# Performance work log

Measured on AMD Instinct MI355X. Metric: run time of the kernel, lower is better.

Reference implementation:

```python
import jax, jax.numpy as jnp
import numpy as np

N_NODES = 100000

def gcn_conv(x, src, dst, W, b, n):
    # PyG GCNConv: h = W x; add self-loops; norm = d^-1/2[src] * d^-1/2[dst]; scatter-add at dst; + b
    h = x @ W
    loop = jnp.arange(n, dtype=src.dtype)
    s = jnp.concatenate([src, loop])
    d = jnp.concatenate([dst, loop])
    deg = jax.ops.segment_sum(jnp.ones_like(d, dtype=h.dtype), d, num_segments=n)
    dis = jnp.where(deg > 0, jax.lax.rsqrt(deg), 0.0)
    norm = dis[s] * dis[d]                     # [E+n]
    msg = h[s] * norm[:, None]                  # [E+n, F] big gather
    out = jax.ops.segment_sum(msg, d, num_segments=n)
    return out + b

def setup_inputs() -> dict:
    key = jax.random.key(0)
    ks = jax.random.split(key, 12)
    n, e, f = N_NODES, 3200000, 14
    hid = [64, 64, 32]
    c = 2
    x = jax.random.normal(ks[0], (n, f), dtype=jnp.float32)
    edge_index = jax.random.randint(ks[1], (2, e), 0, n, dtype=jnp.int64)
    batch = jnp.sort(jax.random.randint(ks[2], (n,), 0, 2000, dtype=jnp.int64))
    def lin(k, fi, fo):
        s = 1.0 / np.sqrt(fi)
        return jax.random.uniform(k, (fi, fo), jnp.float32, -s, s)
    W1 = lin(ks[3], f, hid[0]); b1 = jnp.zeros((hid[0],), jnp.float32)
    W2 = lin(ks[4], hid[0], hid[1]); b2 = jnp.zeros((hid[1],), jnp.float32)
    W3 = lin(ks[5], hid[1], hid[2]); b3 = jnp.zeros((hid[2],), jnp.float32)
    W4 = lin(ks[6], hid[2], c); b4 = jnp.zeros((c,), jnp.float32)
    return {"x": x, "edge_index": edge_index, "batch": batch, "num_graphs": 2000,
            "W1": W1, "b1": b1, "W2": W2, "b2": b2, "W3": W3, "b3": b3, "W4": W4, "b4": b4}

def reference(x, edge_index, batch, num_graphs, W1, b1, W2, b2, W3, b3, W4, b4):
    n = x.shape[0]
    src, dst = edge_index[0], edge_index[1]
    h = jax.nn.relu(gcn_conv(x, src, dst, W1, b1, n))   # dropout = identity at inference
    h = jax.nn.relu(gcn_conv(h, src, dst, W2, b2, n))
    h = jax.nn.relu(gcn_conv(h, src, dst, W3, b3, n))
    h = gcn_conv(h, src, dst, W4, b4, n)
    # global mean pool over graphs
    sums = jax.ops.segment_sum(h, batch, num_segments=num_graphs)
    cnts = jax.ops.segment_sum(jnp.ones((n,), h.dtype), batch, num_segments=num_graphs)
    pooled = sums / jnp.maximum(cnts, 1.0)[:, None]
    return jax.nn.log_softmax(pooled, axis=-1)
```

## Files before the change

kernel.cpp:

```cpp
#include <hip/hip_runtime.h>
#include <hip/hip_fp16.h>
#include <math.h>
#include <type_traits>

static constexpr int THREADS = 256;
static constexpr int CAP   = 80;
static constexpr int BSH   = 9;
static constexpr int SUBS  = 4;
static constexpr int SUBN  = 128;
static constexpr int CAPB  = 17920;
static constexpr int MAXB  = 256;


__global__ void k_zero_i(int* __restrict__ p, int n) {
    int i = blockIdx.x * blockDim.x + threadIdx.x;
    if (i < n) p[i] = 0;
}


__global__ __launch_bounds__(THREADS)
void k_part(const int* __restrict__ src, const int* __restrict__ dst,
            int* __restrict__ bcnt, int* __restrict__ pairs, int e, int nbuck) {
    __shared__ int hist[MAXB];
    __shared__ int base_s[MAXB];
    for (int i = threadIdx.x; i < nbuck; i += THREADS) hist[i] = 0;
    __syncthreads();

    int i0 = (blockIdx.x * THREADS + (int)threadIdx.x) * 8;
    int ss[8], dd[8], bb[8], rk[8];
    int c8 = 0;
    if (i0 < e) {
        c8 = min(8, e - i0);
        if (c8 == 8) {
            int4 d0 = ((const int4*)(dst + i0))[0];
            int4 d1 = ((const int4*)(dst + i0))[1];
            int4 s0 = ((const int4*)(src + i0))[0];
            int4 s1 = ((const int4*)(src + i0))[1];
            dd[0]=d0.x; dd[1]=d0.y; dd[2]=d0.z; dd[3]=d0.w;
            dd[4]=d1.x; dd[5]=d1.y; dd[6]=d1.z; dd[7]=d1.w;
            ss[0]=s0.x; ss[1]=s0.y; ss[2]=s0.z; ss[3]=s0.w;
            ss[4]=s1.x; ss[5]=s1.y; ss[6]=s1.z; ss[7]=s1.w;
        } else {
            for (int j = 0; j < c8; ++j) { dd[j] = dst[i0 + j]; ss[j] = src[i0 + j]; }
        }
        for (int j = 0; j < c8; ++j) {
            bb[j] = dd[j] >> BSH;
            rk[j] = atomicAdd(&hist[bb[j]], 1);
        }
    }
    __syncthreads();
    for (int i = threadIdx.x; i < nbuck; i += THREADS)
        base_s[i] = hist[i] ? atomicAdd(&bcnt[i], hist[i]) : 0;
    __syncthreads();
    for (int j = 0; j < c8; ++j) {
        int idx = base_s[bb[j]] + rk[j];
        if (idx < CAPB)
            pairs[(size_t)bb[j] * CAPB + idx] = ((dd[j] & ((1 << BSH) - 1)) << 17) | ss[j];
    }
}


__global__ __launch_bounds__(THREADS)
void k_scat2(const int* __restrict__ pairs, const int* __restrict__ bcnt,
             int* __restrict__ cnt, int* __restrict__ csr, int n) {
    __shared__ int slab[SUBN * CAP];
    __shared__ int lcnt[SUBN];
    int bucket = blockIdx.x / SUBS;
    int sub    = blockIdx.x % SUBS;
    int gnode0 = (bucket << BSH) + sub * SUBN;
    if (gnode0 >= n) return;
    for (int i = threadIdx.x; i < SUBN; i += THREADS) lcnt[i] = 0;
    __syncthreads();

    int m = min(bcnt[bucket], CAPB);
    const int* pp = pairs + (size_t)bucket * CAPB;
    for (int i0 = (int)threadIdx.x * 4; i0 < m; i0 += THREADS * 4) {
        int k = min(4, m - i0);
        int v[4];
        if (k == 4) {
            int4 a = *(const int4*)(pp + i0);
            v[0] = a.x; v[1] = a.y; v[2] = a.z; v[3] = a.w;
        } else {
            for (int j = 0; j < k; ++j) v[j] = pp[i0 + j];
        }
#pragma unroll
        for (int j = 0; j < 4; ++j) {
            if (j < k) {
                int dl = v[j] >> 17;
                if ((dl >> 7) == sub) {
                    int ln = dl & (SUBN - 1);
                    int p = atomicAdd(&lcnt[ln], 1);
                    if (p < CAP) slab[ln * CAP + p] = v[j] & 0x1FFFF;
                }
            }
        }
    }
    __syncthreads();

    size_t gbase = (size_t)gnode0 * CAP;
    for (int idx = threadIdx.x; idx < SUBN * CAP; idx += THREADS) {
        int node = gnode0 + idx / CAP;
        if (node < n) csr[gbase + idx] = slab[idx];
    }
    for (int i = threadIdx.x; i < SUBN; i += THREADS) {
        int node = gnode0 + i;
        if (node < n) cnt[node] = min(lcnt[i], CAP);
    }
}


__global__ __launch_bounds__(THREADS)
void k_dis_xs(const int* __restrict__ deg, const float* __restrict__ x,
              float* __restrict__ dis, __half2* __restrict__ xs, int n) {
    int i = blockIdx.x * blockDim.x + threadIdx.x;
    if (i >= n) return;
    float dn = rsqrtf((float)(deg[i] + 1));
    dis[i] = dn;
    const float* xr = x + (size_t)i * 14;
    __half2* o = xs + (size_t)i * 8;
#pragma unroll
    for (int fl = 0; fl < 7; ++fl) {
        float2 v;
        v.x = dn * xr[fl * 2];
        v.y = dn * xr[fl * 2 + 1];
        o[fl] = __float22half2_rn(v);
    }
    o[7] = __float22half2_rn(make_float2(0.f, 0.f));
}


template<int SG, int HPL, bool SELF_SCALE, bool EPI_SCALE, bool BIAS, bool RELU>
__global__ __launch_bounds__(THREADS)
void k_gather_pk(const __half2* __restrict__ hw, const int* __restrict__ deg,
                 const int* __restrict__ csr, const float* __restrict__ dis,
                 const float* __restrict__ bias, float* __restrict__ out, int n) {
    constexpr int RS = SG * HPL;
    int tid = blockIdx.x * THREADS + threadIdx.x;
    int node = tid / SG;
    int fl = tid % SG;
    if (node >= n) return;
    size_t o = (size_t)node * CAP;
    int dg = deg[node];
    float dn = dis[node];

    auto loadrow = [&](int s, __half2* r) {
        const __half2* p = hw + (size_t)s * RS + fl * HPL;
        if constexpr (HPL == 4) {
            union { uint4 u; __half2 h[4]; } t;
            t.u = *(const uint4*)p;
            r[0] = t.h[0]; r[1] = t.h[1]; r[2] = t.h[2]; r[3] = t.h[3];
        } else if constexpr (HPL == 2) {
            union { uint2 u; __half2 h[2]; } t;
            t.u = *(const uint2*)p;
            r[0] = t.h[0]; r[1] = t.h[1];
        } else {
            r[0] = *p;
        }
    };

    float2 self[HPL];
    {
        __half2 r[HPL];
        loadrow(node, r);
#pragma unroll
        for (int q = 0; q < HPL; ++q) {
            self[q] = __half22float2(r[q]);
            if (SELF_SCALE) { self[q].x *= dn; self[q].y *= dn; }
        }
    }

    __half2 z = __float2half2_rn(0.f);
    __half2 c0[HPL], c1[HPL], c2[HPL], c3[HPL];
#pragma unroll
    for (int q = 0; q < HPL; ++q) { c0[q] = z; c1[q] = z; c2[q] = z; c3[q] = z; }

    int base = 0;
    for (; base + SG <= dg; base += SG) {
        int cs = csr[o + base + fl];
#pragma unroll
        for (int t = 0; t < SG; t += 4) {
            int s0 = __shfl(cs, t, SG),     s1 = __shfl(cs, t + 1, SG);
            int s2 = __shfl(cs, t + 2, SG), s3 = __shfl(cs, t + 3, SG);
            __half2 r0[HPL], r1[HPL], r2[HPL], r3[HPL];
            loadrow(s0, r0); loadrow(s1, r1); loadrow(s2, r2); loadrow(s3, r3);
#pragma unroll
            for (int q = 0; q < HPL; ++q) {
                c0[q] = __hadd2(c0[q], r0[q]);
                c1[q] = __hadd2(c1[q], r1[q]);
                c2[q] = __hadd2(c2[q], r2[q]);
                c3[q] = __hadd2(c3[q], r3[q]);
            }
        }
    }
    int rem = dg - base;
    if (rem > 0) {
        int cs = (fl < rem) ? csr[o + base + fl] : 0;
        int t = 0;
        for (; t + 4 <= rem; t += 4) {
            int s0 = __shfl(cs, t, SG),     s1 = __shfl(cs, t + 1, SG);
            int s2 = __shfl(cs, t + 2, SG), s3 = __shfl(cs, t + 3, SG);
            __half2 r0[HPL], r1[HPL], r2[HPL], r3[HPL];
            loadrow(s0, r0); loadrow(s1, r1); loadrow(s2, r2); loadrow(s3, r3);
#pragma unroll
            for (int q = 0; q < HPL; ++q) {
                c0[q] = __hadd2(c0[q], r0[q]);
                c1[q] = __hadd2(c1[q], r1[q]);
                c2[q] = __hadd2(c2[q], r2[q]);
                c3[q] = __hadd2(c3[q], r3[q]);
            }
        }
        for (; t < rem; ++t) {
            int s = __shfl(cs, t, SG);
            __half2 r[HPL];
            loadrow(s, r);
#pragma unroll
            for (int q = 0; q < HPL; ++q) c0[q] = __hadd2(c0[q], r[q]);
        }
    }

    float* op = out + (size_t)node * 2 * RS + fl * 2 * HPL;
#pragma unroll
    for (int q = 0; q < HPL; ++q) {
        float2 v0 = __half22float2(c0[q]), v1 = __half22float2(c1[q]);
        float2 v2 = __half22float2(c2[q]), v3 = __half22float2(c3[q]);
        float2 v;
        v.x = self[q].x + (v0.x + v1.x) + (v2.x + v3.x);
        v.y = self[q].y + (v0.y + v1.y) + (v2.y + v3.y);
        if (EPI_SCALE) { v.x *= dn; v.y *= dn; }
        if (BIAS) {
            float2 b = ((const float2*)bias)[fl * HPL + q];
            v.x += b.x; v.y += b.y;
        }
        if (RELU) { v.x = fmaxf(v.x, 0.f); v.y = fmaxf(v.y, 0.f); }
        op[q * 2 + 0] = v.x;
        op[q * 2 + 1] = v.y;
    }
}


__global__ __launch_bounds__(THREADS)
void k_gather_l3(const __half2* __restrict__ hw, const int* __restrict__ deg,
                 const int* __restrict__ csr, const float* __restrict__ dis,
                 const float* __restrict__ b3, const float* __restrict__ W4,
                 float2* __restrict__ hw4, int n) {
    constexpr int SG = 4, HPL = 4, RS = 16;
    __shared__ float Ws4[64];
    if (threadIdx.x < 64) Ws4[threadIdx.x] = W4[threadIdx.x];
    __syncthreads();

    int tid = blockIdx.x * THREADS + threadIdx.x;
    int node = tid / SG;
    int fl = tid % SG;
    if (node >= n) return;
    size_t o = (size_t)node * CAP;
    int dg = deg[node];
    float dn = dis[node];

    auto loadrow = [&](int s, __half2* r) {
        union { uint4 u; __half2 h[4]; } t;
        t.u = *(const uint4*)(hw + (size_t)s * RS + fl * HPL);
        r[0] = t.h[0]; r[1] = t.h[1]; r[2] = t.h[2]; r[3] = t.h[3];
    };

    float2 self[HPL];
    {
        __half2 r[HPL];
        loadrow(node, r);
#pragma unroll
        for (int q = 0; q < HPL; ++q) self[q] = __half22float2(r[q]);
    }

    __half2 z = __float2half2_rn(0.f);
    __half2 c0[HPL], c1[HPL], c2[HPL], c3[HPL];
#pragma unroll
    for (int q = 0; q < HPL; ++q) { c0[q] = z; c1[q] = z; c2[q] = z; c3[q] = z; }

    int base = 0;
    for (; base + SG <= dg; base += SG) {
        int cs = csr[o + base + fl];
#pragma unroll
        for (int t = 0; t < SG; t += 4) {
            int s0 = __shfl(cs, t, SG),     s1 = __shfl(cs, t + 1, SG);
            int s2 = __shfl(cs, t + 2, SG), s3 = __shfl(cs, t + 3, SG);
            __half2 r0[HPL], r1[HPL], r2[HPL], r3[HPL];
            loadrow(s0, r0); loadrow(s1, r1); loadrow(s2, r2); loadrow(s3, r3);
#pragma unroll
            for (int q = 0; q < HPL; ++q) {
                c0[q] = __hadd2(c0[q], r0[q]);
                c1[q] = __hadd2(c1[q], r1[q]);
                c2[q] = __hadd2(c2[q], r2[q]);
                c3[q] = __hadd2(c3[q], r3[q]);
            }
        }
    }
    int rem = dg - base;
    if (rem > 0) {
        int cs = (fl < rem) ? csr[o + base + fl] : 0;
        for (int t = 0; t < rem; ++t) {
            int s = __shfl(cs, t, SG);
            __half2 r[HPL];
            loadrow(s, r);
#pragma unroll
            for (int q = 0; q < HPL; ++q) c0[q] = __hadd2(c0[q], r[q]);
        }
    }

    float p0 = 0.f, p1 = 0.f;
#pragma unroll
    for (int q = 0; q < HPL; ++q) {
        float2 v0 = __half22float2(c0[q]), v1 = __half22float2(c1[q]);
        float2 v2 = __half22float2(c2[q]), v3 = __half22float2(c3[q]);
        float2 v;
        v.x = self[q].x + (v0.x + v1.x) + (v2.x + v3.x);
        v.y = self[q].y + (v0.y + v1.y) + (v2.y + v3.y);
        v.x *= dn; v.y *= dn;
        float2 b = ((const float2*)b3)[fl * HPL + q];
        v.x = fmaxf(v.x + b.x, 0.f);
        v.y = fmaxf(v.y + b.y, 0.f);
        int f = 8 * fl + 2 * q;
        p0 += v.x * Ws4[f * 2 + 0] + v.y * Ws4[(f + 1) * 2 + 0];
        p1 += v.x * Ws4[f * 2 + 1] + v.y * Ws4[(f + 1) * 2 + 1];
    }
    p0 += __shfl_xor(p0, 1, SG); p0 += __shfl_xor(p0, 2, SG);
    p1 += __shfl_xor(p1, 1, SG); p1 += __shfl_xor(p1, 2, SG);
    if (fl == 0) hw4[node] = make_float2(p0 * dn, p1 * dn);
}


__global__ __launch_bounds__(THREADS)
void k_gather2p(const float2* __restrict__ hw, const int* __restrict__ deg,
                const int* __restrict__ csr, const float* __restrict__ dis,
                const float* __restrict__ b, const int* __restrict__ batch,
                float* __restrict__ sums, float* __restrict__ cnts, int n) {
    int tid = blockIdx.x * blockDim.x + threadIdx.x;
    int node = tid >> 3, fl = tid & 7;
    if (node >= n) return;
    size_t o = (size_t)node * CAP;
    int dg = deg[node];
    float x0 = 0.f, y0 = 0.f, x1 = 0.f, y1 = 0.f;
    for (int base = 0; base < dg; base += 32) {
        int idx0 = base + 4 * fl;
        int ldx = min(idx0, CAP - 4);
        int4 c4 = *(const int4*)(csr + o + ldx);
#pragma unroll
        for (int q = 0; q < 4; ++q) {
            bool ok = (idx0 + q) < dg;
            int s = ok ? (&c4.x)[q] : node;
            float2 v = hw[s];
            if (ok) {
                if (q & 1) { x1 += v.x; y1 += v.y; }
                else       { x0 += v.x; y0 += v.y; }
            }
        }
    }
    float sx = x0 + x1, sy = y0 + y1;
    sx += __shfl_xor(sx, 1, 8); sx += __shfl_xor(sx, 2, 8); sx += __shfl_xor(sx, 4, 8);
    sy += __shfl_xor(sy, 1, 8); sy += __shfl_xor(sy, 2, 8); sy += __shfl_xor(sy, 4, 8);
    if (fl == 0) {
        float2 a = hw[node];
        float dn = dis[node];
        float h0 = (a.x + sx) * dn + b[0];
        float h1 = (a.y + sy) * dn + b[1];
        int g = batch[node];
        atomicAdd(&sums[g * 2 + 0], h0);
        atomicAdd(&sums[g * 2 + 1], h1);
        atomicAdd(&cnts[g], 1.0f);
    }
}


template<int KW, int K, int KSTR, int FOUT, bool EPI_BIAS_RELU, typename OUT_T>
__global__ __launch_bounds__(THREADS)
void k_gemm_rb(const float* __restrict__ in, const float* __restrict__ W,
               const float* __restrict__ dis, const float* __restrict__ bias,
               OUT_T* __restrict__ out, int n) {
    constexpr int CG = FOUT / 4;
    __shared__ float Ws[K * FOUT];
    for (int i = threadIdx.x; i < K * FOUT; i += THREADS) {
        int r = i / FOUT;
        Ws[i] = (r < KW) ? W[i] : 0.0f;
    }
    __syncthreads();
    int gid = blockIdx.x * THREADS + threadIdx.x;
    int pair = gid / CG, cg = gid % CG;
    int node0 = pair * 2;
    if (node0 >= n) return;
    bool two = (node0 + 1 < n);
    const float4* r0 = (const float4*)(in + (size_t)node0 * KSTR);
    const float4* r1 = two ? (const float4*)(in + (size_t)(node0 + 1) * KSTR) : r0;
    const float4* Wf4 = (const float4*)Ws;
    float4 acc0 = {0.f, 0.f, 0.f, 0.f}, acc1 = {0.f, 0.f, 0.f, 0.f};
#pragma unroll
    for (int k0 = 0; k0 < K / 4; ++k0) {
        float4 x0 = r0[k0];
        float4 x1 = r1[k0];
#pragma unroll
        for (int kk = 0; kk < 4; ++kk) {
            float4 wv = Wf4[(k0 * 4 + kk) * CG + cg];
            float a = (&x0.x)[kk], b = (&x1.x)[kk];
            acc0.x += a * wv.x; acc0.y += a * wv.y; acc0.z += a * wv.z; acc0.w += a * wv.w;
            acc1.x += b * wv.x; acc1.y += b * wv.y; acc1.z += b * wv.z; acc1.w += b * wv.w;
        }
    }
    float dn0 = dis[node0];
    float dn1 = two ? dis[node0 + 1] : 0.f;
    acc0.x *= dn0; acc0.y *= dn0; acc0.z *= dn0; acc0.w *= dn0;
    acc1.x *= dn1; acc1.y *= dn1; acc1.z *= dn1; acc1.w *= dn1;
    if (EPI_BIAS_RELU) {
        float4 bv = ((const float4*)bias)[cg];
        acc0.x = fmaxf(acc0.x + bv.x, 0.f); acc0.y = fmaxf(acc0.y + bv.y, 0.f);
        acc0.z = fmaxf(acc0.z + bv.z, 0.f); acc0.w = fmaxf(acc0.w + bv.w, 0.f);
        acc1.x = fmaxf(acc1.x + bv.x, 0.f); acc1.y = fmaxf(acc1.y + bv.y, 0.f);
        acc1.z = fmaxf(acc1.z + bv.z, 0.f); acc1.w = fmaxf(acc1.w + bv.w, 0.f);
    }
    if constexpr (std::is_same<OUT_T, __half>::value) {
        union { __half2 h[2]; uint2 u; } p0, p1;
        p0.h[0] = __floats2half2_rn(acc0.x, acc0.y);
        p0.h[1] = __floats2half2_rn(acc0.z, acc0.w);
        *(uint2*)(out + (size_t)node0 * FOUT + cg * 4) = p0.u;
        if (two) {
            p1.h[0] = __floats2half2_rn(acc1.x, acc1.y);
            p1.h[1] = __floats2half2_rn(acc1.z, acc1.w);
            *(uint2*)(out + (size_t)(node0 + 1) * FOUT + cg * 4) = p1.u;
        }
    } else {
        ((float4*)(out + (size_t)node0 * FOUT))[cg] = acc0;
        if (two) ((float4*)(out + (size_t)(node0 + 1) * FOUT))[cg] = acc1;
    }
}


__global__ void k_zero2(float* __restrict__ sums, float* __restrict__ cnts, int ng) {
    int i = blockIdx.x * blockDim.x + threadIdx.x;
    if (i < ng) {
        sums[i * 2 + 0] = 0.0f;
        sums[i * 2 + 1] = 0.0f;
        cnts[i] = 0.0f;
    }
}

__global__ void k_logsoftmax(const float* __restrict__ sums, const float* __restrict__ cnts,
                             float* __restrict__ out, int ng) {
    int g = blockIdx.x * blockDim.x + threadIdx.x;
    if (g >= ng) return;
    float c = fmaxf(cnts[g], 1.0f);
    float p0 = sums[g * 2 + 0] / c;
    float p1 = sums[g * 2 + 1] / c;
    float m = fmaxf(p0, p1);
    float l = m + logf(expf(p0 - m) + expf(p1 - m));
    out[g * 2 + 0] = p0 - l;
    out[g * 2 + 1] = p1 - l;
}


static inline int nblk(long long t) { return (int)((t + THREADS - 1) / THREADS); }

extern "C" void kernel_launch(void* const* d_in, const int* in_sizes, int n_in,
                              void* d_out, int out_size, void* d_ws, size_t ws_size,
                              hipStream_t stream) {
    const float* x     = (const float*)d_in[0];
    const int*   ei    = (const int*)d_in[1];
    const int*   batch = (const int*)d_in[2];
    const float* W1 = (const float*)d_in[4];
    const float* b1 = (const float*)d_in[5];
    const float* W2 = (const float*)d_in[6];
    const float* b2 = (const float*)d_in[7];
    const float* W3 = (const float*)d_in[8];
    const float* b3 = (const float*)d_in[9];
    const float* W4 = (const float*)d_in[10];
    const float* b4 = (const float*)d_in[11];

    const int n  = in_sizes[0] / 14;
    const int e  = in_sizes[1] / 2;
    const int ng = out_size / 2;
    const int* src = ei;
    const int* dst = ei + e;
    const int nb = nblk(n);
    const int nbuck = (n + (1 << BSH) - 1) >> BSH;

    char* ws = (char*)d_ws;
    size_t off_b = 0;
    auto alloc = [&](size_t bytes) -> char* {
        char* p = ws + off_b;
        off_b = (off_b + bytes + 255) & ~(size_t)255;
        return p;
    };
    int*     cnt  = (int*)alloc((size_t)n * 4);
    int*     bcnt = (int*)alloc((size_t)MAXB * 4);
    float*   dis  = (float*)alloc((size_t)n * 4);
    int*     csr  = (int*)alloc((size_t)n * CAP * 4);
    __half2* xs16 = (__half2*)alloc((size_t)n * 8 * 4);
    float*   agg1 = (float*)alloc((size_t)n * 16 * 4);
    float*   hbuf = (float*)alloc((size_t)n * 64 * 4);
    __half2* hw16 = (__half2*)alloc((size_t)n * 32 * 4);
    float*   hw4  = (float*)alloc((size_t)n * 2 * 4);
    float*   sums = (float*)alloc((size_t)ng * 2 * 4);
    float*   cnts = (float*)alloc((size_t)ng * 4);
    int*     pairs = (int*)hbuf;
    (void)ws_size; (void)n_in;

    k_zero_i<<<1, THREADS, 0, stream>>>(bcnt, MAXB);
    k_part<<<nblk(((long long)e + 7) / 8), THREADS, 0, stream>>>(src, dst, bcnt, pairs, e, nbuck);
    k_scat2<<<nbuck * SUBS, THREADS, 0, stream>>>(pairs, bcnt, cnt, csr, n);
    k_dis_xs<<<nb, THREADS, 0, stream>>>(cnt, x, dis, xs16, n);

    k_gather_pk<4, 2, true, false, false, false><<<nblk((long long)n * 4), THREADS, 0, stream>>>(
        xs16, cnt, csr, dis, nullptr, agg1, n);
    k_gemm_rb<14, 16, 16, 64, true, float><<<nblk((long long)(n / 2 + 1) * 16), THREADS, 0, stream>>>(
        agg1, W1, dis, b1, hbuf, n);

    k_gemm_rb<64, 64, 64, 64, false, __half><<<nblk((long long)(n / 2 + 1) * 16), THREADS, 0, stream>>>(
        hbuf, W2, dis, nullptr, (__half*)hw16, n);
    k_gather_pk<8, 4, false, true, true, true><<<nblk((long long)n * 8), THREADS, 0, stream>>>(
        hw16, cnt, csr, dis, b2, hbuf, n);

    k_gemm_rb<64, 64, 64, 32, false, __half><<<nblk((long long)(n / 2 + 1) * 8), THREADS, 0, stream>>>(
        hbuf, W3, dis, nullptr, (__half*)hw16, n);
    k_gather_l3<<<nblk((long long)n * 4), THREADS, 0, stream>>>(
        hw16, cnt, csr, dis, b3, W4, (float2*)hw4, n);

    k_zero2<<<nblk(ng), THREADS, 0, stream>>>(sums, cnts, ng);
    k_gather2p<<<nblk((long long)n * 8), THREADS, 0, stream>>>(
        (const float2*)hw4, cnt, csr, dis, b4, batch, sums, cnts, n);
    k_logsoftmax<<<nblk(ng), THREADS, 0, stream>>>(sums, cnts, (float*)d_out, ng);
}
```

Measured before the change: 369.5 us.

## Replace last-layer CSR gather with bucketed pair scan and segmented pooling

The final GCN layer aggregation now reads the destination-bucketed edge pairs left over from partitioning, rather than the padded CSR. Each block covers half a bucket, accumulates the 2-wide messages in shared memory with atomics, then does a run-length segmented reduction over the sorted batch ids so far fewer global atomics hit the pooled sums. The pairs buffer gets its own workspace allocation instead of aliasing hbuf, so it survives until the last layer. In exchange, each block scans the whole bucket (both halves read every pair) and leans on shared-memory atomic contention.

```diff
diff --git a/kernel.cpp b/kernel.cpp
--- a/kernel.cpp
+++ b/kernel.cpp
@@ -10,6 +10,7 @@
 static constexpr int SUBN  = 128;
 static constexpr int CAPB  = 17920;
 static constexpr int MAXB  = 256;
+static constexpr int L4WN  = 256;
 
 
 __global__ void k_zero_i(int* __restrict__ p, int n) {
@@ -328,104 +329,75 @@
 
 
 __global__ __launch_bounds__(THREADS)
-void k_gather2p(const float2* __restrict__ hw, const int* __restrict__ deg,
-                const int* __restrict__ csr, const float* __restrict__ dis,
-                const float* __restrict__ b, const int* __restrict__ batch,
-                float* __restrict__ sums, float* __restrict__ cnts, int n) {
-    int tid = blockIdx.x * blockDim.x + threadIdx.x;
-    int node = tid >> 3, fl = tid & 7;
-    if (node >= n) return;
-    size_t o = (size_t)node * CAP;
-    int dg = deg[node];
-    float x0 = 0.f, y0 = 0.f, x1 = 0.f, y1 = 0.f;
-    for (int base = 0; base < dg; base += 32) {
-        int idx0 = base + 4 * fl;
-        int ldx = min(idx0, CAP - 4);
-        int4 c4 = *(const int4*)(csr + o + ldx);
-#pragma unroll
-        for (int q = 0; q < 4; ++q) {
-            bool ok = (idx0 + q) < dg;
-            int s = ok ? (&c4.x)[q] : node;
-            float2 v = hw[s];
-            if (ok) {
-                if (q & 1) { x1 += v.x; y1 += v.y; }
-                else       { x0 += v.x; y0 += v.y; }
+void k_l4pool(const int* __restrict__ pairs, const int* __restrict__ bcnt,
+              const float2* __restrict__ hw4, const float* __restrict__ dis,
+              const float* __restrict__ b4, const int* __restrict__ batch,
+              float* __restrict__ sums, float* __restrict__ cnts, int n) {
+    __shared__ float accx[L4WN], accy[L4WN];
+    int bucket = blockIdx.x >> 1;
+    int sub    = blockIdx.x & 1;
+    int gnode0 = (bucket << BSH) + sub * L4WN;
+    if (gnode0 >= n) return;
+    for (int i = threadIdx.x; i < L4WN; i += THREADS) { accx[i] = 0.f; accy[i] = 0.f; }
+    __syncthreads();
+
+    int m = min(bcnt[bucket], CAPB);
+    const int* pp = pairs + (size_t)bucket * CAPB;
+    for (int i0 = (int)threadIdx.x * 4; i0 < m; i0 += THREADS * 4) {
+        int k = min(4, m - i0);
+        int v[4];
+        if (k == 4) {
+            int4 a = *(const int4*)(pp + i0);
+            v[0] = a.x; v[1] = a.y; v[2] = a.z; v[3] = a.w;
+        } else {
+            for (int j = 0; j < k; ++j) v[j] = pp[i0 + j];
+        }
+        float2 w[4]; int ln[4]; bool ok[4];
+#pragma unroll
+        for (int j = 0; j < 4; ++j) {
+            int dl = v[j] >> 17;
+            ok[j] = (j < k) && ((dl >> 8) == sub);
+            ln[j] = dl & (L4WN - 1);
+            int s = ok[j] ? (v[j] & 0x1FFFF) : 0;
+            w[j] = hw4[s];
+        }
+#pragma unroll
+        for (int j = 0; j < 4; ++j) {
+            if (ok[j]) {
+                atomicAdd(&accx[ln[j]], w[j].x);
+                atomicAdd(&accy[ln[j]], w[j].y);
             }
         }
     }
-    float sx = x0 + x1, sy = y0 + y1;
-    sx += __shfl_xor(sx, 1, 8); sx += __shfl_xor(sx, 2, 8); sx += __shfl_xor(sx, 4, 8);
-    sy += __shfl_xor(sy, 1, 8); sy += __shfl_xor(sy, 2, 8); sy += __shfl_xor(sy, 4, 8);
-    if (fl == 0) {
-        float2 a = hw[node];
-        float dn = dis[node];
-        float h0 = (a.x + sx) * dn + b[0];
-        float h1 = (a.y + sy) * dn + b[1];
-        int g = batch[node];
-        atomicAdd(&sums[g * 2 + 0], h0);
-        atomicAdd(&sums[g * 2 + 1], h1);
-        atomicAdd(&cnts[g], 1.0f);
-    }
-}
-
-
-template<int KW, int K, int KSTR, int FOUT, bool EPI_BIAS_RELU, typename OUT_T>
-__global__ __launch_bounds__(THREADS)
-void k_gemm_rb(const float* __restrict__ in, const float* __restrict__ W,
-               const float* __restrict__ dis, const float* __restrict__ bias,
-               OUT_T* __restrict__ out, int n) {
-    constexpr int CG = FOUT / 4;
-    __shared__ float Ws[K * FOUT];
-    for (int i = threadIdx.x; i < K * FOUT; i += THREADS) {
-        int r = i / FOUT;
-        Ws[i] = (r < KW) ? W[i] : 0.0f;
-    }
-    __syncthreads();
-    int gid = blockIdx.x * THREADS + threadIdx.x;
-    int pair = gid / CG, cg = gid % CG;
-    int node0 = pair * 2;
-    if (node0 >= n) return;
-    bool two = (node0 + 1 < n);
-    const float4* r0 = (const float4*)(in + (size_t)node0 * KSTR);
-    const float4* r1 = two ? (const float4*)(in + (size_t)(node0 + 1) * KSTR) : r0;
-    const float4* Wf4 = (const float4*)Ws;
-    float4 acc0 = {0.f, 0.f, 0.f, 0.f}, acc1 = {0.f, 0.f, 0.f, 0.f};
-#pragma unroll
-    for (int k0 = 0; k0 < K / 4; ++k0) {
-        float4 x0 = r0[k0];
-        float4 x1 = r1[k0];
-#pragma unroll
-        for (int kk = 0; kk < 4; ++kk) {
-            float4 wv = Wf4[(k0 * 4 + kk) * CG + cg];
-            float a = (&x0.x)[kk], b = (&x1.x)[kk];
-            acc0.x += a * wv.x; acc0.y += a * wv.y; acc0.z += a * wv.z; acc0.w += a * wv.w;
-            acc1.x += b * wv.x; acc1.y += b * wv.y; acc1.z += b * wv.z; acc1.w += b * wv.w;
-        }
-    }
-    float dn0 = dis[node0];
-    float dn1 = two ? dis[node0 + 1] : 0.f;
-    acc0.x *= dn0; acc0.y *= dn0; acc0.z *= dn0; acc0.w *= dn0;
-    acc1.x *= dn1; acc1.y *= dn1; acc1.z *= dn1; acc1.w *= dn1;
-    if (EPI_BIAS_RELU) {
-        float4 bv = ((const float4*)bias)[cg];
-        acc0.x = fmaxf(acc0.x + bv.x, 0.f); acc0.y = fmaxf(acc0.y + bv.y, 0.f);
-        acc0.z = fmaxf(acc0.z + bv.z, 0.f); acc0.w = fmaxf(acc0.w + bv.w, 0.f);
-        acc1.x = fmaxf(acc1.x + bv.x, 0.f); acc1.y = fmaxf(acc1.y + bv.y, 0.f);
-        acc1.z = fmaxf(acc1.z + bv.z, 0.f); acc1.w = fmaxf(acc1.w + bv.w, 0.f);
-    }
-    if constexpr (std::is_same<OUT_T, __half>::value) {
-        union { __half2 h[2]; uint2 u; } p0, p1;
-        p0.h[0] = __floats2half2_rn(acc0.x, acc0.y);
-        p0.h[1] = __floats2half2_rn(acc0.z, acc0.w);
-        *(uint2*)(out + (size_t)node0 * FOUT + cg * 4) = p0.u;
-        if (two) {
-            p1.h[0] = __floats2half2_rn(acc1.x, acc1.y);
-            p1.h[1] = __floats2half2_rn(acc1.z, acc1.w);
-            *(uint2*)(out + (size_t)(node0 + 1) * FOUT + cg * 4) = p1.u;
-        }
-    } else {
-        ((float4*)(out + (size_t)node0 * FOUT))[cg] = acc0;
-        if (two) ((float4*)(out + (size_t)(node0 + 1) * FOUT))[cg] = acc1;
+    __syncthreads();
+
+    if (threadIdx.x < L4WN / 8) {
+        int i0 = threadIdx.x * 8;
+        int nvalid = min(gnode0 + L4WN, n) - gnode0;
+        int end = min(i0 + 8, nvalid);
+        if (i0 < nvalid) {
+            float bx = b4[0], by = b4[1];
+            int g = batch[gnode0 + i0];
+            float v0 = 0.f, v1 = 0.f, c = 0.f;
+            for (int i = i0; i < end; ++i) {
+                int node = gnode0 + i;
+                int gi = batch[node];
+                if (gi != g) {
+                    atomicAdd(&sums[g * 2 + 0], v0);
+                    atomicAdd(&sums[g * 2 + 1], v1);
+                    atomicAdd(&cnts[g], c);
+                    g = gi; v0 = 0.f; v1 = 0.f; c = 0.f;
+                }
+                float2 self = hw4[node];
+                float dn = dis[node];
+                v0 += (self.x + accx[i]) * dn + bx;
+                v1 += (self.y + accy[i]) * dn + by;
+                c += 1.0f;
+            }
+            atomicAdd(&sums[g * 2 + 0], v0);
+            atomicAdd(&sums[g * 2 + 1], v1);
+            atomicAdd(&cnts[g], c);
+        }
     }
 }
 
@@ -450,6 +422,67 @@
     float l = m + logf(expf(p0 - m) + expf(p1 - m));
     out[g * 2 + 0] = p0 - l;
     out[g * 2 + 1] = p1 - l;
+}
+
+
+template<int KW, int K, int KSTR, int FOUT, bool EPI_BIAS_RELU, typename OUT_T>
+__global__ __launch_bounds__(THREADS)
+void k_gemm_rb(const float* __restrict__ in, const float* __restrict__ W,
+               const float* __restrict__ dis, const float* __restrict__ bias,
+               OUT_T* __restrict__ out, int n) {
+    constexpr int CG = FOUT / 4;
+    __shared__ float Ws[K * FOUT];
+    for (int i = threadIdx.x; i < K * FOUT; i += THREADS) {
+        int r = i / FOUT;
+        Ws[i] = (r < KW) ? W[i] : 0.0f;
+    }
+    __syncthreads();
+    int gid = blockIdx.x * THREADS + threadIdx.x;
+    int pair = gid / CG, cg = gid % CG;
+    int node0 = pair * 2;
+    if (node0 >= n) return;
+    bool two = (node0 + 1 < n);
+    const float4* r0 = (const float4*)(in + (size_t)node0 * KSTR);
+    const float4* r1 = two ? (const float4*)(in + (size_t)(node0 + 1) * KSTR) : r0;
+    const float4* Wf4 = (const float4*)Ws;
+    float4 acc0 = {0.f, 0.f, 0.f, 0.f}, acc1 = {0.f, 0.f, 0.f, 0.f};
+#pragma unroll
+    for (int k0 = 0; k0 < K / 4; ++k0) {
+        float4 x0 = r0[k0];
+        float4 x1 = r1[k0];
+#pragma unroll
+        for (int kk = 0; kk < 4; ++kk) {
+            float4 wv = Wf4[(k0 * 4 + kk) * CG + cg];
+            float a = (&x0.x)[kk], b = (&x1.x)[kk];
+            acc0.x += a * wv.x; acc0.y += a * wv.y; acc0.z += a * wv.z; acc0.w += a * wv.w;
+            acc1.x += b * wv.x; acc1.y += b * wv.y; acc1.z += b * wv.z; acc1.w += b * wv.w;
+        }
+    }
+    float dn0 = dis[node0];
+    float dn1 = two ? dis[node0 + 1] : 0.f;
+    acc0.x *= dn0; acc0.y *= dn0; acc0.z *= dn0; acc0.w *= dn0;
+    acc1.x *= dn1; acc1.y *= dn1; acc1.z *= dn1; acc1.w *= dn1;
+    if (EPI_BIAS_RELU) {
+        float4 bv = ((const float4*)bias)[cg];
+        acc0.x = fmaxf(acc0.x + bv.x, 0.f); acc0.y = fmaxf(acc0.y + bv.y, 0.f);
+        acc0.z = fmaxf(acc0.z + bv.z, 0.f); acc0.w = fmaxf(acc0.w + bv.w, 0.f);
+        acc1.x = fmaxf(acc1.x + bv.x, 0.f); acc1.y = fmaxf(acc1.y + bv.y, 0.f);
+        acc1.z = fmaxf(acc1.z + bv.z, 0.f); acc1.w = fmaxf(acc1.w + bv.w, 0.f);
+    }
+    if constexpr (std::is_same<OUT_T, __half>::value) {
+        union { __half2 h[2]; uint2 u; } p0, p1;
+        p0.h[0] = __floats2half2_rn(acc0.x, acc0.y);
+        p0.h[1] = __floats2half2_rn(acc0.z, acc0.w);
+        *(uint2*)(out + (size_t)node0 * FOUT + cg * 4) = p0.u;
+        if (two) {
+            p1.h[0] = __floats2half2_rn(acc1.x, acc1.y);
+            p1.h[1] = __floats2half2_rn(acc1.z, acc1.w);
+            *(uint2*)(out + (size_t)(node0 + 1) * FOUT + cg * 4) = p1.u;
+        }
+    } else {
+        ((float4*)(out + (size_t)node0 * FOUT))[cg] = acc0;
+        if (two) ((float4*)(out + (size_t)(node0 + 1) * FOUT))[cg] = acc1;
+    }
 }
 
 
@@ -489,6 +522,7 @@
     int*     bcnt = (int*)alloc((size_t)MAXB * 4);
     float*   dis  = (float*)alloc((size_t)n * 4);
     int*     csr  = (int*)alloc((size_t)n * CAP * 4);
+    int*     pairs= (int*)alloc((size_t)nbuck * CAPB * 4);
     __half2* xs16 = (__half2*)alloc((size_t)n * 8 * 4);
     float*   agg1 = (float*)alloc((size_t)n * 16 * 4);
     float*   hbuf = (float*)alloc((size_t)n * 64 * 4);
@@ -496,7 +530,6 @@
     float*   hw4  = (float*)alloc((size_t)n * 2 * 4);
     float*   sums = (float*)alloc((size_t)ng * 2 * 4);
     float*   cnts = (float*)alloc((size_t)ng * 4);
-    int*     pairs = (int*)hbuf;
     (void)ws_size; (void)n_in;
 
     k_zero_i<<<1, THREADS, 0, stream>>>(bcnt, MAXB);
@@ -520,7 +553,7 @@
         hw16, cnt, csr, dis, b3, W4, (float2*)hw4, n);
 
     k_zero2<<<nblk(ng), THREADS, 0, stream>>>(sums, cnts, ng);
-    k_gather2p<<<nblk((long long)n * 8), THREADS, 0, stream>>>(
-        (const float2*)hw4, cnt, csr, dis, b4, batch, sums, cnts, n);
+    k_l4pool<<<nbuck * 2, THREADS, 0, stream>>>(
+        pairs, bcnt, (const float2*)hw4, dis, b4, batch, sums, cnts, n);
     k_logsoftmax<<<nblk(ng), THREADS, 0, stream>>>(sums, cnts, (float*)d_out, ng);
 }
```

Result: faster. 344.0 us (-6.9%).
